# Performance work log

Hardware: AMD Instinct MI355X
Metric: run time of the kernel (lower is better)

The kernel has to match this reference:

```python
import jax, jax.numpy as jnp
import numpy as np

# sparsity config (from constant.args.sparsity.activation)
N_SP, M_SP = 2, 4      # first-level n:m (keep n of every m channels)
N2_SP, M2_SP = 1, 8    # second-level n2:m2 applied to the residual


def _nm_mask(xa, n, m):
    """Per-block top-n mask over channel blocks of size m.
    xa: non-negative magnitudes, shape (N, C, H, W).
    Keeps entries >= the n-th largest value in each block (ties kept,
    matching torch's `b < topk_val` -> 0 semantics)."""
    N, C, H, W = xa.shape
    b = xa.reshape(N, C // m, m, H, W)
    # n-th largest == ascending-sorted index (m - n); keep dim for broadcast
    thr = jnp.sort(b, axis=2)[:, :, m - n : m - n + 1]
    return (b >= thr).reshape(N, C, H, W)


def setup_inputs() -> dict:
    key = jax.random.key(0)
    x = jax.random.normal(key, (64, 256, 56, 56), dtype=jnp.float32)
    return {"x": x}


def reference(x):
    xa = jnp.abs(x)
    mask1 = _nm_mask(xa, N_SP, M_SP)
    # second-level mask: zero out already-kept entries, then top-n2 of m2 blocks
    resid = jnp.where(mask1, jnp.zeros((), xa.dtype), xa)
    mask2 = _nm_mask(resid, N2_SP, M2_SP)
    mask = mask1 | mask2  # torch does mask += mask2 then .bool()
    return x * mask.astype(x.dtype)
```

## Files before the change

### kernel.cpp

```cpp
#include <hip/hip_runtime.h>


#define N_IMG   64
#define C_CH    256
#define HW      3136
#define HW4     784
#define CH_OCT  32
#define COLS    (N_IMG * HW4)
#define KCH     4
#define BLK     256

typedef float vfloat4 __attribute__((ext_vector_type(4)));

__device__ __forceinline__ float second_largest4(float a, float b, float c, float d) {
    float mab = fmaxf(a, b), nab = fminf(a, b);
    float mcd = fmaxf(c, d), ncd = fminf(c, d);
    return fmaxf(fminf(mab, mcd), fmaxf(nab, ncd));
}

__device__ __forceinline__ void mask_oct(vfloat4 v[8]) {
    #pragma unroll
    for (int e = 0; e < 4; ++e) {
        float a[8];
        #pragma unroll
        for (int c = 0; c < 8; ++c) a[c] = fabsf(v[c][e]);

        const float thr1a = second_largest4(a[0], a[1], a[2], a[3]);
        const float thr1b = second_largest4(a[4], a[5], a[6], a[7]);

        float res[8];
        bool  m1[8];
        #pragma unroll
        for (int c = 0; c < 4; ++c) { m1[c] = a[c] >= thr1a; res[c] = m1[c] ? 0.0f : a[c]; }
        #pragma unroll
        for (int c = 4; c < 8; ++c) { m1[c] = a[c] >= thr1b; res[c] = m1[c] ? 0.0f : a[c]; }

        float thr2 = res[0];
        #pragma unroll
        for (int c = 1; c < 8; ++c) thr2 = fmaxf(thr2, res[c]);

        #pragma unroll
        for (int c = 0; c < 8; ++c) {
            const bool keep = m1[c] | (res[c] >= thr2);
            v[c][e] = keep ? v[c][e] : 0.0f;
        }
    }
}

__global__ __launch_bounds__(BLK) void sparsity_kernel(const float* __restrict__ x,
                                                       float* __restrict__ out) {
    const int cb   = blockIdx.y;
    const int col0 = blockIdx.x * (BLK * KCH) + threadIdx.x;

    size_t base[KCH];
    #pragma unroll
    for (int k = 0; k < KCH; ++k) {
        const int col = col0 + k * BLK;
        const int n   = col / HW4;
        const int hw4 = col - n * HW4;
        base[k] = (size_t)n * (C_CH * HW) + (size_t)cb * (8 * HW) + (size_t)hw4 * 4;
    }

    vfloat4 cur[8], nxt[8];

    {
        const vfloat4* px = (const vfloat4*)(x + base[0]);
        #pragma unroll
        for (int c = 0; c < 8; ++c)
            cur[c] = __builtin_nontemporal_load(&px[c * (HW / 4)]);
    }

    #pragma unroll
    for (int k = 0; k < KCH; ++k) {
        if (k + 1 < KCH) {
            const vfloat4* px = (const vfloat4*)(x + base[k + 1]);
            #pragma unroll
            for (int c = 0; c < 8; ++c)
                nxt[c] = __builtin_nontemporal_load(&px[c * (HW / 4)]);
        }

        mask_oct(cur);

        {
            vfloat4* po = (vfloat4*)(out + base[k]);
            #pragma unroll
            for (int c = 0; c < 8; ++c)
                __builtin_nontemporal_store(cur[c], &po[c * (HW / 4)]);
        }

        #pragma unroll
        for (int c = 0; c < 8; ++c) cur[c] = nxt[c];
    }
}

extern "C" void kernel_launch(void* const* d_in, const int* in_sizes, int n_in,
                              void* d_out, int out_size, void* d_ws, size_t ws_size,
                              hipStream_t stream) {
    const float* x = (const float*)d_in[0];
    float* out = (float*)d_out;
    dim3 grid(COLS / (BLK * KCH), CH_OCT);
    sparsity_kernel<<<grid, 256, 0, stream>>>(x, out);
}
```

Before: 336.6 us.

## Switch to persistent grid with one block per CU via shared-memory ballast

```diff
diff --git a/kernel.cpp b/kernel.cpp
--- a/kernel.cpp
+++ b/kernel.cpp
@@ -7,7 +7,10 @@
 #define HW4     784
 #define CH_OCT  32
 #define COLS    (N_IMG * HW4)
-#define KCH     4
+#define CBLK    196
+#define STEPS   6272
+#define NBLK    224
+#define SPB     28
 #define BLK     256
 
 typedef float vfloat4 __attribute__((ext_vector_type(4)));
@@ -47,49 +50,53 @@
     }
 }
 
+__device__ __forceinline__ size_t step_base(int s, int t) {
+    const int cb   = s / CBLK;
+    const int col  = (s - cb * CBLK) * BLK + t;
+    const int n    = col / HW4;
+    const int hw4  = col - n * HW4;
+    return (size_t)n * (C_CH * HW4) + (size_t)cb * (8 * HW4) + (size_t)hw4;
+}
+
 __global__ __launch_bounds__(BLK) void sparsity_kernel(const float* __restrict__ x,
                                                        float* __restrict__ out) {
-    const int cb   = blockIdx.y;
-    const int col0 = blockIdx.x * (BLK * KCH) + threadIdx.x;
+    __shared__ float ballast[25600];
+    if ((size_t)x == 1) ballast[threadIdx.x] = 0.0f;
 
-    size_t base[KCH];
-    #pragma unroll
-    for (int k = 0; k < KCH; ++k) {
-        const int col = col0 + k * BLK;
-        const int n   = col / HW4;
-        const int hw4 = col - n * HW4;
-        base[k] = (size_t)n * (C_CH * HW) + (size_t)cb * (8 * HW) + (size_t)hw4 * 4;
-    }
+    const int t  = threadIdx.x;
+    const int s0 = blockIdx.x * SPB;
+
+    const vfloat4* gx = (const vfloat4*)x;
+    vfloat4*       go = (vfloat4*)out;
 
     vfloat4 cur[8], nxt[8];
 
     {
-        const vfloat4* px = (const vfloat4*)(x + base[0]);
+        const size_t b = step_base(s0, t);
         #pragma unroll
         for (int c = 0; c < 8; ++c)
-            cur[c] = __builtin_nontemporal_load(&px[c * (HW / 4)]);
+            cur[c] = __builtin_nontemporal_load(&gx[b + (size_t)c * HW4]);
     }
 
-    #pragma unroll
-    for (int k = 0; k < KCH; ++k) {
-        if (k + 1 < KCH) {
-            const vfloat4* px = (const vfloat4*)(x + base[k + 1]);
+    size_t bcur = step_base(s0, t);
+    for (int i = 0; i < SPB; ++i) {
+        size_t bnxt = 0;
+        if (i + 1 < SPB) {
+            bnxt = step_base(s0 + i + 1, t);
             #pragma unroll
             for (int c = 0; c < 8; ++c)
-                nxt[c] = __builtin_nontemporal_load(&px[c * (HW / 4)]);
+                nxt[c] = __builtin_nontemporal_load(&gx[bnxt + (size_t)c * HW4]);
         }
 
         mask_oct(cur);
 
-        {
-            vfloat4* po = (vfloat4*)(out + base[k]);
-            #pragma unroll
-            for (int c = 0; c < 8; ++c)
-                __builtin_nontemporal_store(cur[c], &po[c * (HW / 4)]);
-        }
+        #pragma unroll
+        for (int c = 0; c < 8; ++c)
+            __builtin_nontemporal_store(cur[c], &go[bcur + (size_t)c * HW4]);
 
         #pragma unroll
         for (int c = 0; c < 8; ++c) cur[c] = nxt[c];
+        bcur = bnxt;
     }
 }
 
@@ -98,6 +105,5 @@
                               hipStream_t stream) {
     const float* x = (const float*)d_in[0];
     float* out = (float*)d_out;
-    dim3 grid(COLS / (BLK * KCH), CH_OCT);
-    sparsity_kernel<<<grid, 256, 0, stream>>>(x, out);
+    sparsity_kernel<<<dim3(NBLK), dim3(BLK), 0, stream>>>(x, out);
 }
```

New measurement: 331.3 us. About the same (-1.6%).
